# Optimization experiments

Measured on AMD Instinct MI355X. Metric: run time of the kernel, lower is better.

Reference implementation:

```python
import jax, jax.numpy as jnp
import numpy as np
from jax import lax

P, T, A = 4096, 128, 32
K = int(P * 0.1)          # elite count = 409
TEMP, MOM, MIN_STD = 0.5, 0.1, 0.05
INF = jnp.float32(1e30)   # large finite stand-in for +inf (grad-safe)


def setup_inputs() -> dict:
    key = jax.random.key(0)
    k1, k2 = jax.random.split(key)
    obs_diffs = jax.random.uniform(k1, (P, T, T), dtype=jnp.float32)  # pairwise MSE costs >= 0
    means = jnp.zeros((T, 1, A), dtype=jnp.float32)
    stds = jnp.ones((T, 1, A), dtype=jnp.float32)
    noise = jax.random.normal(k2, (T, P, A), dtype=jnp.float32)
    return {"obs_diffs": obs_diffs, "means": means, "stds": stds, "noise": noise}


def _dtw_dists(obs_diffs):
    """DTW-style min-plus DP: D[i+1,j+1] = min(D[i,j+1], D[i+1,j], D[i,j]) + c[i,j].
    obs_diffs: [P, T, T] -> dists: [P] (= D[:, T, T])."""
    p = obs_diffs.shape[0]
    inf_col = jnp.full((p,), INF, dtype=obs_diffs.dtype)
    # row 0 of the (T+1)x(T+1) table: [0, inf, inf, ...]
    row0 = jnp.concatenate([jnp.zeros((p, 1), obs_diffs.dtype),
                            jnp.full((p, obs_diffs.shape[1]), INF, obs_diffs.dtype)], axis=1)

    def row_step(prev_row, c_row):  # prev_row [P, T+1], c_row [P, T]
        def inner(carry, xs):        # carry = new[j] (left neighbor), vectorized over P
            p_j1, p_j, c = xs        # prev[j+1], prev[j], cost  -- each [P]
            new = jnp.minimum(jnp.minimum(p_j1, p_j), carry) + c
            return new, new
        xs = (prev_row[:, 1:].T, prev_row[:, :-1].T, c_row.T)  # each [T, P]
        _, vals = lax.scan(inner, inf_col, xs)                  # vals [T, P]
        new_row = jnp.concatenate([inf_col[:, None], vals.T], axis=1)
        return new_row, None

    final_row, _ = lax.scan(row_step, row0, jnp.swapaxes(obs_diffs, 0, 1))
    return final_row[:, -1]


def reference(obs_diffs, means, stds, noise):
    # sample population of action trajectories
    actions = jnp.clip(means + stds * noise, -1.0, 1.0)        # [T, P, A]
    dists = _dtw_dists(obs_diffs)                               # [P]
    neg_top, idxs = lax.top_k(-dists, K)                        # K smallest dists
    elite_diffs = -neg_top                                      # [K]
    elite_actions = actions[:, idxs]                            # [T, K, A]
    min_diff = elite_diffs.min()
    score = jnp.exp(TEMP * (min_diff - elite_diffs))
    score = score / score.sum()
    ssum = score.sum()                                          # == 1, kept to match torch
    w = score[None, :, None]                                    # [1, K, 1]
    _mean = jnp.sum(w * elite_actions, axis=1, keepdims=True) / (ssum + 1e-9)   # [T,1,A]
    _std = jnp.sqrt(jnp.sum(w * (elite_actions - _mean) ** 2, axis=1, keepdims=True) / (ssum + 1e-9))
    _std = jnp.clip(_std, MIN_STD, 1.0)
    means_new = MOM * means + (1.0 - MOM) * _mean
    return jnp.stack([means_new, _std])                         # [2, T, 1, A]
```

## Files before the change

kernel.cpp:

```cpp
#include <hip/hip_runtime.h>
#include <math.h>

#define P_N 4096
#define T_N 128
#define A_N 32
#define K_N 409
#define TEMP_C 0.5f
#define MOM_C 0.1f
#define MIN_STD_C 0.05f
#define INF_F 1e30f

typedef float vfloat4 __attribute__((ext_vector_type(4)));

#define DPPMOV(dst, src, ctrl, oldv)                                          \
  {                                                                           \
    union { float f; int i; } _a, _b, _r;                                     \
    _a.f = (src); _b.f = (oldv);                                              \
    _r.i = __builtin_amdgcn_update_dpp(_b.i, _a.i, (ctrl), 0xF, 0xF, false);  \
    (dst) = _r.f;                                                             \
  }

__global__ __launch_bounds__(256) void dtw_kernel(const float* __restrict__ obs,
                                                  float* __restrict__ dists) {
  const int tid  = threadIdx.x;
  const int wave = tid >> 6;
  const int lane = tid & 63;
  const int half = lane >> 5;
  const int l    = lane & 31;
  const int p    = blockIdx.x * 8 + wave * 2 + half;
  const bool is0 = (l == 0);

  const vfloat4* row = (const vfloat4*)(obs + (size_t)p * (T_N * T_N)) + l;

  float P1 = INF_F, P2 = INF_F, P3 = INF_F, P4 = INF_F;
  float p0 = is0 ? 0.0f : INF_F;

  vfloat4 cb[8];
  #pragma unroll
  for (int u = 0; u < 8; ++u) cb[u] = __builtin_nontemporal_load(row + u * 32);

  for (int rb = 0; rb < T_N; rb += 8) {
    const bool pf = (rb + 8 < T_N);
    #pragma unroll
    for (int u = 0; u < 8; ++u) {
      vfloat4 c = cb[u];
      if (pf) cb[u] = __builtin_nontemporal_load(row + (rb + u + 8) * 32);

      float a1 = fminf(P1, p0);
      float a2 = fminf(P2, P1);
      float a3 = fminf(P3, P2);
      float a4 = fminf(P4, P3);

      float B = a1 + c.x;
      B = fminf(B + c.y, a2 + c.y);
      B = fminf(B + c.z, a3 + c.z);
      B = fminf(B + c.w, a4 + c.w);
      float C = (c.x + c.y) + (c.z + c.w);

      float Bp, Cp;
      DPPMOV(Bp, B, 0x111, INF_F); DPPMOV(Cp, C, 0x111, 0.0f);
      B = fminf(Bp + C, B); C = Cp + C;
      DPPMOV(Bp, B, 0x112, INF_F); DPPMOV(Cp, C, 0x112, 0.0f);
      B = fminf(Bp + C, B); C = Cp + C;
      DPPMOV(Bp, B, 0x114, INF_F); DPPMOV(Cp, C, 0x114, 0.0f);
      B = fminf(Bp + C, B); C = Cp + C;
      DPPMOV(Bp, B, 0x118, INF_F); DPPMOV(Cp, C, 0x118, 0.0f);
      B = fminf(Bp + C, B); C = Cp + C;
      DPPMOV(Bp, B, 0x142, INF_F); DPPMOV(Cp, C, 0x142, 0.0f);
      B = fminf(Bp + C, B); C = Cp + C;

      float x;
      DPPMOV(x, B, 0x138, INF_F);
      x = is0 ? INF_F : x;

      float n1 = fminf(a1, x)  + c.x;
      float n2 = fminf(a2, n1) + c.y;
      float n3 = fminf(a3, n2) + c.z;
      float n4 = fminf(a4, n3) + c.w;

      p0 = x; P1 = n1; P2 = n2; P3 = n3; P4 = n4;
    }
  }

  if (l == 31) dists[p] = P4;
}

#define HSTRIDE 257

__global__ __launch_bounds__(1024) void select_kernel(const float* __restrict__ dists,
                                                      int* __restrict__ elite_idx,
                                                      float* __restrict__ elite_wn,
                                                      float* __restrict__ meta) {
  __shared__ alignas(16) unsigned int skey[P_N];
  __shared__ unsigned int histw[16 * HSTRIDE];
  __shared__ float elite_d[K_N];
  __shared__ int eqbuf[256];
  __shared__ float wsum[16];
  __shared__ unsigned int sc_prefix, sc_minkey;
  __shared__ int sc_r, sc_cntlt, sc_cnteq;
  __shared__ float sS, sS2;

  const int tid  = threadIdx.x;
  const int wid  = tid >> 6;
  const int lane = tid & 63;

  const float4 d4 = ((const float4*)dists)[tid];
  const unsigned int ka = __float_as_uint(d4.x);
  const unsigned int kb = __float_as_uint(d4.y);
  const unsigned int kc = __float_as_uint(d4.z);
  const unsigned int kd = __float_as_uint(d4.w);
  ((uint4*)skey)[tid] = make_uint4(ka, kb, kc, kd);
  unsigned int localmin = ka;
  if (kb < localmin) localmin = kb;
  if (kc < localmin) localmin = kc;
  if (kd < localmin) localmin = kd;
  #pragma unroll
  for (int d = 32; d > 0; d >>= 1) {
    unsigned int o = __shfl_xor(localmin, (unsigned)d, 64);
    if (o < localmin) localmin = o;
  }
  if (tid == 0) { sc_minkey = 0xFFFFFFFFu; sc_cntlt = 0; sc_cnteq = 0;
                  sc_prefix = 0; sc_r = K_N - 1; }
  __syncthreads();
  if (lane == 0) atomicMin(&sc_minkey, localmin);
  __syncthreads();

  unsigned int mask = 0;
  for (int shift = 24; shift >= 0; shift -= 8) {
    for (int b = tid; b < 16 * HSTRIDE; b += 1024) histw[b] = 0;
    __syncthreads();
    unsigned int pref = sc_prefix;
    for (int p = tid; p < P_N; p += 1024) {
      unsigned int k = skey[p];
      if ((k & mask) == pref)
        atomicAdd(&histw[wid * HSTRIDE + ((k >> shift) & 255u)], 1u);
    }
    __syncthreads();
    if (tid < 256) {
      unsigned tot = 0;
      #pragma unroll
      for (int w = 0; w < 16; ++w) tot += histw[w * HSTRIDE + tid];
      histw[tid] = tot;
    }
    __syncthreads();
    if (tid < 64) {
      unsigned h0 = histw[tid * 4 + 0], h1 = histw[tid * 4 + 1];
      unsigned h2 = histw[tid * 4 + 2], h3 = histw[tid * 4 + 3];
      unsigned s1 = h0 + h1, s2 = s1 + h2, s3 = s2 + h3;
      unsigned tot = s3;
      #pragma unroll
      for (int d = 1; d < 64; d <<= 1) {
        unsigned o = __shfl_up(tot, (unsigned)d, 64);
        if (tid >= d) tot += o;
      }
      unsigned base = tot - s3;
      unsigned rr = (unsigned)sc_r;
      if (rr >= base && rr < base + s3) {
        int bsel; unsigned lo;
        if (rr < base + h0)      { bsel = 0; lo = base; }
        else if (rr < base + s1) { bsel = 1; lo = base + h0; }
        else if (rr < base + s2) { bsel = 2; lo = base + s1; }
        else                     { bsel = 3; lo = base + s2; }
        sc_prefix |= (unsigned)(tid * 4 + bsel) << shift;
        sc_r = (int)(rr - lo);
      }
    }
    mask |= 0xFFu << shift;
    __syncthreads();
  }

  const unsigned int tk = sc_prefix;
  const int needeq = sc_r + 1;

  for (int p = tid; p < P_N; p += 1024) {
    unsigned int k = skey[p];
    const bool lt = (k < tk);
    unsigned long long m = __ballot(lt);
    int base = 0;
    if (lane == 0) base = atomicAdd(&sc_cntlt, (int)__popcll(m));
    base = __shfl(base, 0, 64);
    if (lt) {
      int pos = base + (int)__popcll(m & ((1ull << lane) - 1ull));
      elite_idx[pos] = p;
      elite_d[pos]   = __uint_as_float(k);
    } else if (k == tk) {
      int ep = atomicAdd(&sc_cnteq, 1);
      if (ep < 256) eqbuf[ep] = p;
    }
  }
  __syncthreads();
  if (tid == 0) {
    int cl = sc_cntlt;
    int ce = sc_cnteq; if (ce > 256) ce = 256;
    for (int rsel = 0; rsel < needeq; ++rsel) {
      int best = 0x7FFFFFFF, bi = 0;
      for (int m = 0; m < ce; ++m) {
        int v = eqbuf[m];
        if (v < best) { best = v; bi = m; }
      }
      eqbuf[bi] = 0x7FFFFFFF;
      elite_idx[cl + rsel] = best;
      elite_d[cl + rsel]   = __uint_as_float(tk);
    }
  }
  __syncthreads();

  const float minf = __uint_as_float(sc_minkey);
  float s = (tid < K_N) ? expf(TEMP_C * (minf - elite_d[tid])) : 0.0f;
  float t1 = s;
  #pragma unroll
  for (int d = 32; d > 0; d >>= 1) t1 += __shfl_xor(t1, (unsigned)d, 64);
  if (lane == 0) wsum[wid] = t1;
  __syncthreads();
  if (tid == 0) {
    float acc = 0.0f;
    #pragma unroll
    for (int w = 0; w < 16; ++w) acc += wsum[w];
    sS = acc;
  }
  __syncthreads();
  const float S = sS;
  const float wn = (tid < K_N) ? (s / S) : 0.0f;
  float t2 = wn;
  #pragma unroll
  for (int d = 32; d > 0; d >>= 1) t2 += __shfl_xor(t2, (unsigned)d, 64);
  if (lane == 0) wsum[wid] = t2;
  __syncthreads();
  if (tid == 0) {
    float acc = 0.0f;
    #pragma unroll
    for (int w = 0; w < 16; ++w) acc += wsum[w];
    sS2 = acc;
  }
  __syncthreads();
  if (tid < K_N) elite_wn[tid] = wn;
  if (tid == 0) meta[0] = sS2;
}

__global__ __launch_bounds__(512) void elite_stats_kernel(
    const float* __restrict__ noise, const float* __restrict__ means,
    const float* __restrict__ stds, const int* __restrict__ elite_idx,
    const float* __restrict__ elite_wn, const float* __restrict__ meta,
    float* __restrict__ out) {
  const int t = blockIdx.x;
  const int tid = threadIdx.x;
  const int a  = tid & 31;
  const int er = tid >> 5;
  __shared__ int   sidx[K_N];
  __shared__ float swn[K_N];
  __shared__ float sM[16][32];
  __shared__ float sQ[16][32];

  for (int e = tid; e < K_N; e += 512) { sidx[e] = elite_idx[e]; swn[e] = elite_wn[e]; }
  __syncthreads();

  const float mn = means[t * A_N + a];
  const float sd = stds[t * A_N + a];
  const float* nrow = noise + (size_t)t * P_N * A_N;

  float M = 0.0f, Q = 0.0f;
  for (int e = er; e < K_N; e += 16) {
    const int idx = sidx[e];
    const float w = swn[e];
    float x = mn + sd * nrow[idx * A_N + a];
    x = fminf(1.0f, fmaxf(-1.0f, x));
    M += w * x;
    Q += w * x * x;
  }
  sM[er][a] = M; sQ[er][a] = Q;
  __syncthreads();

  if (tid < 32) {
    float Ms = 0.0f, Qs = 0.0f;
    #pragma unroll
    for (int r = 0; r < 16; ++r) { Ms += sM[r][a]; Qs += sQ[r][a]; }
    const float ssum = meta[0];
    const float D = ssum + 1e-9f;
    const float mu = Ms / D;
    float var = (Qs - 2.0f * mu * Ms + mu * mu * ssum) / D;
    float stdv = sqrtf(fmaxf(var, 0.0f));
    stdv = fminf(1.0f, fmaxf(MIN_STD_C, stdv));
    out[t * A_N + a]              = MOM_C * mn + (1.0f - MOM_C) * mu;
    out[T_N * A_N + t * A_N + a]  = stdv;
  }
}

extern "C" void kernel_launch(void* const* d_in, const int* in_sizes, int n_in,
                              void* d_out, int out_size, void* d_ws, size_t ws_size,
                              hipStream_t stream) {
  const float* obs   = (const float*)d_in[0];
  const float* means = (const float*)d_in[1];
  const float* stds  = (const float*)d_in[2];
  const float* noise = (const float*)d_in[3];
  float* out = (float*)d_out;

  float* dists     = (float*)d_ws;
  int*   elite_idx = (int*)(dists + P_N);
  float* elite_wn  = (float*)(elite_idx + 512);
  float* meta      = elite_wn + 512;

  dtw_kernel<<<P_N / 8, 256, 0, stream>>>(obs, dists);
  select_kernel<<<1, 1024, 0, stream>>>(dists, elite_idx, elite_wn, meta);
  elite_stats_kernel<<<T_N, 512, 0, stream>>>(noise, means, stds,
                                              elite_idx, elite_wn, meta, out);
}
```

Measured before the change: 400.5 us.

## Fuse DTW, elite selection and stats into one flag-synchronized kernel

Merges the DTW, top-k selection and elite statistics kernels into a single launch of 256 blocks. Blocks hand off to each other through agent-scope done flags: the last block runs the selection once every DTW block has finished, and the first 128 blocks wait for it before computing the per-timestep stats. The radix select also skips leading bytes shared by the min and max keys, and uses ballot-aggregated histogram atomics. This removes inter-kernel launch gaps and some histogram work, but it depends on all blocks being co-resident and adds spin-wait overhead.

Result: slower. 533.9 us (+33.3%).

```diff
diff --git a/kernel.cpp b/kernel.cpp
--- a/kernel.cpp
+++ b/kernel.cpp
@@ -10,6 +10,14 @@
 #define MIN_STD_C 0.05f
 #define INF_F 1e30f
 
+#define NBLK 256
+#define NTHR 512
+#define NW   8
+#define HSTRIDE 257
+#define MAGIC_A 0x9E3779B1u
+#define MAGIC_B 0xC2B2AE35u
+#define SCOPE_AGT __HIP_MEMORY_SCOPE_AGENT
+
 typedef float vfloat4 __attribute__((ext_vector_type(4)));
 
 #define DPPMOV(dst, src, ctrl, oldv)                                          \
@@ -20,268 +28,322 @@
     (dst) = _r.f;                                                             \
   }
 
-__global__ __launch_bounds__(256) void dtw_kernel(const float* __restrict__ obs,
-                                                  float* __restrict__ dists) {
+union Shm {
+  struct {
+    unsigned int skey[P_N];
+    unsigned int histw[NW * HSTRIDE];
+    float elite_d[K_N];
+    int eqbuf[256];
+    float wsum[NW];
+  } sel;
+  struct {
+    int   sidx[K_N];
+    float swn[K_N];
+    float sM[16][32];
+    float sQ[16][32];
+  } st;
+};
+
+__global__ __launch_bounds__(NTHR, 2) void fused_kernel(
+    const float* __restrict__ obs, const float* __restrict__ means,
+    const float* __restrict__ stds, const float* __restrict__ noise,
+    float* __restrict__ dists, int* __restrict__ elite_idx,
+    float* __restrict__ elite_wn, float* __restrict__ meta,
+    unsigned int* __restrict__ done, float* __restrict__ out) {
+  __shared__ Shm shm;
+  __shared__ unsigned int sc_prefix, sc_minkey, sc_maxkey;
+  __shared__ int sc_r, sc_cntlt, sc_cnteq;
+  __shared__ float sS, sS2;
+
+  const int bid  = blockIdx.x;
   const int tid  = threadIdx.x;
   const int wave = tid >> 6;
   const int lane = tid & 63;
-  const int half = lane >> 5;
-  const int l    = lane & 31;
-  const int p    = blockIdx.x * 8 + wave * 2 + half;
-  const bool is0 = (l == 0);
-
-  const vfloat4* row = (const vfloat4*)(obs + (size_t)p * (T_N * T_N)) + l;
-
-  float P1 = INF_F, P2 = INF_F, P3 = INF_F, P4 = INF_F;
-  float p0 = is0 ? 0.0f : INF_F;
-
-  vfloat4 cb[8];
-  #pragma unroll
-  for (int u = 0; u < 8; ++u) cb[u] = __builtin_nontemporal_load(row + u * 32);
-
-  for (int rb = 0; rb < T_N; rb += 8) {
-    const bool pf = (rb + 8 < T_N);
+
+  {
+    const int half = lane >> 5;
+    const int l    = lane & 31;
+    const int p    = bid * 16 + wave * 2 + half;
+    const bool is0 = (l == 0);
+
+    const vfloat4* row = (const vfloat4*)(obs + (size_t)p * (T_N * T_N)) + l;
+
+    float P1 = INF_F, P2 = INF_F, P3 = INF_F, P4 = INF_F;
+    float p0 = is0 ? 0.0f : INF_F;
+
+    vfloat4 cb[8];
     #pragma unroll
-    for (int u = 0; u < 8; ++u) {
-      vfloat4 c = cb[u];
-      if (pf) cb[u] = __builtin_nontemporal_load(row + (rb + u + 8) * 32);
-
-      float a1 = fminf(P1, p0);
-      float a2 = fminf(P2, P1);
-      float a3 = fminf(P3, P2);
-      float a4 = fminf(P4, P3);
-
-      float B = a1 + c.x;
-      B = fminf(B + c.y, a2 + c.y);
-      B = fminf(B + c.z, a3 + c.z);
-      B = fminf(B + c.w, a4 + c.w);
-      float C = (c.x + c.y) + (c.z + c.w);
-
-      float Bp, Cp;
-      DPPMOV(Bp, B, 0x111, INF_F); DPPMOV(Cp, C, 0x111, 0.0f);
-      B = fminf(Bp + C, B); C = Cp + C;
-      DPPMOV(Bp, B, 0x112, INF_F); DPPMOV(Cp, C, 0x112, 0.0f);
-      B = fminf(Bp + C, B); C = Cp + C;
-      DPPMOV(Bp, B, 0x114, INF_F); DPPMOV(Cp, C, 0x114, 0.0f);
-      B = fminf(Bp + C, B); C = Cp + C;
-      DPPMOV(Bp, B, 0x118, INF_F); DPPMOV(Cp, C, 0x118, 0.0f);
-      B = fminf(Bp + C, B); C = Cp + C;
-      DPPMOV(Bp, B, 0x142, INF_F); DPPMOV(Cp, C, 0x142, 0.0f);
-      B = fminf(Bp + C, B); C = Cp + C;
-
-      float x;
-      DPPMOV(x, B, 0x138, INF_F);
-      x = is0 ? INF_F : x;
-
-      float n1 = fminf(a1, x)  + c.x;
-      float n2 = fminf(a2, n1) + c.y;
-      float n3 = fminf(a3, n2) + c.z;
-      float n4 = fminf(a4, n3) + c.w;
-
-      p0 = x; P1 = n1; P2 = n2; P3 = n3; P4 = n4;
-    }
+    for (int u = 0; u < 8; ++u) cb[u] = __builtin_nontemporal_load(row + u * 32);
+
+    for (int rb = 0; rb < T_N; rb += 8) {
+      const bool pf = (rb + 8 < T_N);
+      #pragma unroll
+      for (int u = 0; u < 8; ++u) {
+        vfloat4 c = cb[u];
+        if (pf) cb[u] = __builtin_nontemporal_load(row + (rb + u + 8) * 32);
+
+        float a1 = fminf(P1, p0);
+        float a2 = fminf(P2, P1);
+        float a3 = fminf(P3, P2);
+        float a4 = fminf(P4, P3);
+
+        float B = a1 + c.x;
+        B = fminf(B + c.y, a2 + c.y);
+        B = fminf(B + c.z, a3 + c.z);
+        B = fminf(B + c.w, a4 + c.w);
+        float C = (c.x + c.y) + (c.z + c.w);
+
+        float Bp, Cp;
+        DPPMOV(Bp, B, 0x111, INF_F); DPPMOV(Cp, C, 0x111, 0.0f);
+        B = fminf(Bp + C, B); C = Cp + C;
+        DPPMOV(Bp, B, 0x112, INF_F); DPPMOV(Cp, C, 0x112, 0.0f);
+        B = fminf(Bp + C, B); C = Cp + C;
+        DPPMOV(Bp, B, 0x114, INF_F); DPPMOV(Cp, C, 0x114, 0.0f);
+        B = fminf(Bp + C, B); C = Cp + C;
+        DPPMOV(Bp, B, 0x118, INF_F); DPPMOV(Cp, C, 0x118, 0.0f);
+        B = fminf(Bp + C, B); C = Cp + C;
+        DPPMOV(Bp, B, 0x142, INF_F); DPPMOV(Cp, C, 0x142, 0.0f);
+        B = fminf(Bp + C, B); C = Cp + C;
+
+        float x;
+        DPPMOV(x, B, 0x138, INF_F);
+        x = is0 ? INF_F : x;
+
+        float n1 = fminf(a1, x)  + c.x;
+        float n2 = fminf(a2, n1) + c.y;
+        float n3 = fminf(a3, n2) + c.z;
+        float n4 = fminf(a4, n3) + c.w;
+
+        p0 = x; P1 = n1; P2 = n2; P3 = n3; P4 = n4;
+      }
+    }
+    if (l == 31) dists[p] = P4;
   }
 
-  if (l == 31) dists[p] = P4;
-}
-
-#define HSTRIDE 257
-
-__global__ __launch_bounds__(1024) void select_kernel(const float* __restrict__ dists,
-                                                      int* __restrict__ elite_idx,
-                                                      float* __restrict__ elite_wn,
-                                                      float* __restrict__ meta) {
-  __shared__ alignas(16) unsigned int skey[P_N];
-  __shared__ unsigned int histw[16 * HSTRIDE];
-  __shared__ float elite_d[K_N];
-  __shared__ int eqbuf[256];
-  __shared__ float wsum[16];
-  __shared__ unsigned int sc_prefix, sc_minkey;
-  __shared__ int sc_r, sc_cntlt, sc_cnteq;
-  __shared__ float sS, sS2;
-
-  const int tid  = threadIdx.x;
-  const int wid  = tid >> 6;
-  const int lane = tid & 63;
-
-  const float4 d4 = ((const float4*)dists)[tid];
-  const unsigned int ka = __float_as_uint(d4.x);
-  const unsigned int kb = __float_as_uint(d4.y);
-  const unsigned int kc = __float_as_uint(d4.z);
-  const unsigned int kd = __float_as_uint(d4.w);
-  ((uint4*)skey)[tid] = make_uint4(ka, kb, kc, kd);
-  unsigned int localmin = ka;
-  if (kb < localmin) localmin = kb;
-  if (kc < localmin) localmin = kc;
-  if (kd < localmin) localmin = kd;
-  #pragma unroll
-  for (int d = 32; d > 0; d >>= 1) {
-    unsigned int o = __shfl_xor(localmin, (unsigned)d, 64);
-    if (o < localmin) localmin = o;
+  __threadfence();
+  __syncthreads();
+  if (tid == 0)
+    __hip_atomic_store(&done[bid], MAGIC_A, __ATOMIC_RELEASE, SCOPE_AGT);
+
+  if (bid == NBLK - 1) {
+    if (tid < NBLK) {
+      while (__hip_atomic_load(&done[tid], __ATOMIC_ACQUIRE, SCOPE_AGT) != MAGIC_A)
+        __builtin_amdgcn_s_sleep(8);
+    }
+    __syncthreads();
+    __threadfence();
+
+    if (tid == 0) { sc_minkey = 0xFFFFFFFFu; sc_maxkey = 0u;
+                    sc_cntlt = 0; sc_cnteq = 0; sc_prefix = 0u; sc_r = K_N - 1; }
+    __syncthreads();
+
+    unsigned int localmin = 0xFFFFFFFFu, localmax = 0u;
+    for (int p = tid; p < P_N; p += NTHR) {
+      float dv = __hip_atomic_load(&dists[p], __ATOMIC_RELAXED, SCOPE_AGT);
+      unsigned int k = __float_as_uint(dv);
+      shm.sel.skey[p] = k;
+      if (k < localmin) localmin = k;
+      if (k > localmax) localmax = k;
+    }
+    #pragma unroll
+    for (int d = 32; d > 0; d >>= 1) {
+      unsigned int o = __shfl_xor(localmin, (unsigned)d, 64);
+      if (o < localmin) localmin = o;
+      unsigned int o2 = __shfl_xor(localmax, (unsigned)d, 64);
+      if (o2 > localmax) localmax = o2;
+    }
+    if (lane == 0) { atomicMin(&sc_minkey, localmin); atomicMax(&sc_maxkey, localmax); }
+    __syncthreads();
+    const unsigned int mn = sc_minkey, mx = sc_maxkey;
+
+    unsigned int mask = 0;
+    bool skipping = true;
+    for (int shift = 24; shift >= 0; shift -= 8) {
+      const unsigned int bmin = (mn >> shift) & 255u;
+      const unsigned int bmax = (mx >> shift) & 255u;
+      if (skipping && bmin == bmax) {
+        if (tid == 0) sc_prefix |= bmin << shift;
+        mask |= 0xFFu << shift;
+        __syncthreads();
+        continue;
+      }
+      skipping = false;
+
+      for (int b = tid; b < NW * HSTRIDE; b += NTHR) shm.sel.histw[b] = 0u;
+      __syncthreads();
+      const unsigned int pref = sc_prefix;
+      for (int p = tid; p < P_N; p += NTHR) {
+        unsigned int k  = shm.sel.skey[p];
+        bool act        = ((k & mask) == pref);
+        unsigned int bk = (k >> shift) & 255u;
+        unsigned long long actm = __ballot(act);
+        #pragma unroll
+        for (int it = 0; it < 3; ++it) {
+          if (!actm) break;
+          int ldr = __ffsll((unsigned long long)actm) - 1;
+          unsigned int bl = __shfl(bk, ldr, 64);
+          unsigned long long mm = __ballot(act && (bk == bl));
+          if (act && (lane == ldr))
+            atomicAdd(&shm.sel.histw[wave * HSTRIDE + bl], (unsigned)__popcll(mm));
+          if (act && (bk == bl)) act = false;
+          actm &= ~mm;
+        }
+        if (act) atomicAdd(&shm.sel.histw[wave * HSTRIDE + bk], 1u);
+      }
+      __syncthreads();
+      if (tid < 256) {
+        unsigned int tot = 0;
+        #pragma unroll
+        for (int w = 0; w < NW; ++w) tot += shm.sel.histw[w * HSTRIDE + tid];
+        shm.sel.histw[tid] = tot;
+      }
+      __syncthreads();
+      if (tid < 64) {
+        unsigned h0 = shm.sel.histw[tid * 4 + 0], h1 = shm.sel.histw[tid * 4 + 1];
+        unsigned h2 = shm.sel.histw[tid * 4 + 2], h3 = shm.sel.histw[tid * 4 + 3];
+        unsigned s1 = h0 + h1, s2 = s1 + h2, s3 = s2 + h3;
+        unsigned tot = s3;
+        #pragma unroll
+        for (int d = 1; d < 64; d <<= 1) {
+          unsigned o = __shfl_up(tot, (unsigned)d, 64);
+          if (tid >= d) tot += o;
+        }
+        unsigned base = tot - s3;
+        unsigned rr = (unsigned)sc_r;
+        if (rr >= base && rr < base + s3) {
+          int bsel; unsigned lo;
+          if (rr < base + h0)      { bsel = 0; lo = base; }
+          else if (rr < base + s1) { bsel = 1; lo = base + h0; }
+          else if (rr < base + s2) { bsel = 2; lo = base + s1; }
+          else                     { bsel = 3; lo = base + s2; }
+          sc_prefix |= (unsigned)(tid * 4 + bsel) << shift;
+          sc_r = (int)(rr - lo);
+        }
+      }
+      mask |= 0xFFu << shift;
+      __syncthreads();
+    }
+
+    const unsigned int tk = sc_prefix;
+    const int needeq = sc_r + 1;
+
+    for (int p = tid; p < P_N; p += NTHR) {
+      unsigned int k = shm.sel.skey[p];
+      const bool lt = (k < tk);
+      unsigned long long m = __ballot(lt);
+      int base = 0;
+      if (lane == 0) base = atomicAdd(&sc_cntlt, (int)__popcll(m));
+      base = __shfl(base, 0, 64);
+      if (lt) {
+        int pos = base + (int)__popcll(m & ((1ull << lane) - 1ull));
+        elite_idx[pos]     = p;
+        shm.sel.elite_d[pos] = __uint_as_float(k);
+      } else if (k == tk) {
+        int ep = atomicAdd(&sc_cnteq, 1);
+        if (ep < 256) shm.sel.eqbuf[ep] = p;
+      }
+    }
+    __syncthreads();
+    if (tid == 0) {
+      int cl = sc_cntlt;
+      int ce = sc_cnteq; if (ce > 256) ce = 256;
+      for (int rsel = 0; rsel < needeq; ++rsel) {
+        int best = 0x7FFFFFFF, bi = 0;
+        for (int m = 0; m < ce; ++m) {
+          int v = shm.sel.eqbuf[m];
+          if (v < best) { best = v; bi = m; }
+        }
+        shm.sel.eqbuf[bi] = 0x7FFFFFFF;
+        elite_idx[cl + rsel]     = best;
+        shm.sel.elite_d[cl + rsel] = __uint_as_float(tk);
+      }
+    }
+    __syncthreads();
+
+    const float minf = __uint_as_float(sc_minkey);
+    float s = (tid < K_N) ? expf(TEMP_C * (minf - shm.sel.elite_d[tid])) : 0.0f;
+    float t1 = s;
+    #pragma unroll
+    for (int d = 32; d > 0; d >>= 1) t1 += __shfl_xor(t1, (unsigned)d, 64);
+    if (lane == 0) shm.sel.wsum[wave] = t1;
+    __syncthreads();
+    if (tid == 0) {
+      float acc = 0.0f;
+      #pragma unroll
+      for (int w = 0; w < NW; ++w) acc += shm.sel.wsum[w];
+      sS = acc;
+    }
+    __syncthreads();
+    const float S = sS;
+    const float wn = (tid < K_N) ? (s / S) : 0.0f;
+    float t2 = wn;
+    #pragma unroll
+    for (int d = 32; d > 0; d >>= 1) t2 += __shfl_xor(t2, (unsigned)d, 64);
+    if (lane == 0) shm.sel.wsum[wave] = t2;
+    __syncthreads();
+    if (tid == 0) {
+      float acc = 0.0f;
+      #pragma unroll
+      for (int w = 0; w < NW; ++w) acc += shm.sel.wsum[w];
+      sS2 = acc;
+    }
+    __syncthreads();
+    if (tid < K_N) elite_wn[tid] = wn;
+    if (tid == 0) meta[0] = sS2;
+
+    __threadfence();
+    __syncthreads();
+    if (tid < NBLK)
+      __hip_atomic_store(&done[tid], MAGIC_B, __ATOMIC_RELEASE, SCOPE_AGT);
   }
-  if (tid == 0) { sc_minkey = 0xFFFFFFFFu; sc_cntlt = 0; sc_cnteq = 0;
-                  sc_prefix = 0; sc_r = K_N - 1; }
-  __syncthreads();
-  if (lane == 0) atomicMin(&sc_minkey, localmin);
-  __syncthreads();
-
-  unsigned int mask = 0;
-  for (int shift = 24; shift >= 0; shift -= 8) {
-    for (int b = tid; b < 16 * HSTRIDE; b += 1024) histw[b] = 0;
-    __syncthreads();
-    unsigned int pref = sc_prefix;
-    for (int p = tid; p < P_N; p += 1024) {
-      unsigned int k = skey[p];
-      if ((k & mask) == pref)
-        atomicAdd(&histw[wid * HSTRIDE + ((k >> shift) & 255u)], 1u);
-    }
-    __syncthreads();
-    if (tid < 256) {
-      unsigned tot = 0;
+
+  if (bid < T_N) {
+    if (tid == 0) {
+      while (__hip_atomic_load(&done[bid], __ATOMIC_ACQUIRE, SCOPE_AGT) != MAGIC_B)
+        __builtin_amdgcn_s_sleep(8);
+    }
+    __syncthreads();
+    __threadfence();
+
+    const int t  = bid;
+    const int a  = tid & 31;
+    const int er = tid >> 5;
+
+    for (int e = tid; e < K_N; e += NTHR) {
+      shm.st.sidx[e] = __hip_atomic_load(&elite_idx[e], __ATOMIC_RELAXED, SCOPE_AGT);
+      shm.st.swn[e]  = __hip_atomic_load(&elite_wn[e],  __ATOMIC_RELAXED, SCOPE_AGT);
+    }
+    float ssum_l = __hip_atomic_load(&meta[0], __ATOMIC_RELAXED, SCOPE_AGT);
+    __syncthreads();
+
+    const float mn = means[t * A_N + a];
+    const float sd = stds[t * A_N + a];
+    const float* nrow = noise + (size_t)t * P_N * A_N;
+
+    float M = 0.0f, Q = 0.0f;
+    for (int e = er; e < K_N; e += 16) {
+      const int idx = shm.st.sidx[e];
+      const float w = shm.st.swn[e];
+      float x = mn + sd * nrow[idx * A_N + a];
+      x = fminf(1.0f, fmaxf(-1.0f, x));
+      M += w * x;
+      Q += w * x * x;
+    }
+    shm.st.sM[er][a] = M; shm.st.sQ[er][a] = Q;
+    __syncthreads();
+
+    if (tid < 32) {
+      float Ms = 0.0f, Qs = 0.0f;
       #pragma unroll
-      for (int w = 0; w < 16; ++w) tot += histw[w * HSTRIDE + tid];
-      histw[tid] = tot;
-    }
-    __syncthreads();
-    if (tid < 64) {
-      unsigned h0 = histw[tid * 4 + 0], h1 = histw[tid * 4 + 1];
-      unsigned h2 = histw[tid * 4 + 2], h3 = histw[tid * 4 + 3];
-      unsigned s1 = h0 + h1, s2 = s1 + h2, s3 = s2 + h3;
-      unsigned tot = s3;
-      #pragma unroll
-      for (int d = 1; d < 64; d <<= 1) {
-        unsigned o = __shfl_up(tot, (unsigned)d, 64);
-        if (tid >= d) tot += o;
-      }
-      unsigned base = tot - s3;
-      unsigned rr = (unsigned)sc_r;
-      if (rr >= base && rr < base + s3) {
-        int bsel; unsigned lo;
-        if (rr < base + h0)      { bsel = 0; lo = base; }
-        else if (rr < base + s1) { bsel = 1; lo = base + h0; }
-        else if (rr < base + s2) { bsel = 2; lo = base + s1; }
-        else                     { bsel = 3; lo = base + s2; }
-        sc_prefix |= (unsigned)(tid * 4 + bsel) << shift;
-        sc_r = (int)(rr - lo);
-      }
-    }
-    mask |= 0xFFu << shift;
-    __syncthreads();
-  }
-
-  const unsigned int tk = sc_prefix;
-  const int needeq = sc_r + 1;
-
-  for (int p = tid; p < P_N; p += 1024) {
-    unsigned int k = skey[p];
-    const bool lt = (k < tk);
-    unsigned long long m = __ballot(lt);
-    int base = 0;
-    if (lane == 0) base = atomicAdd(&sc_cntlt, (int)__popcll(m));
-    base = __shfl(base, 0, 64);
-    if (lt) {
-      int pos = base + (int)__popcll(m & ((1ull << lane) - 1ull));
-      elite_idx[pos] = p;
-      elite_d[pos]   = __uint_as_float(k);
-    } else if (k == tk) {
-      int ep = atomicAdd(&sc_cnteq, 1);
-      if (ep < 256) eqbuf[ep] = p;
-    }
-  }
-  __syncthreads();
-  if (tid == 0) {
-    int cl = sc_cntlt;
-    int ce = sc_cnteq; if (ce > 256) ce = 256;
-    for (int rsel = 0; rsel < needeq; ++rsel) {
-      int best = 0x7FFFFFFF, bi = 0;
-      for (int m = 0; m < ce; ++m) {
-        int v = eqbuf[m];
-        if (v < best) { best = v; bi = m; }
-      }
-      eqbuf[bi] = 0x7FFFFFFF;
-      elite_idx[cl + rsel] = best;
-      elite_d[cl + rsel]   = __uint_as_float(tk);
-    }
-  }
-  __syncthreads();
-
-  const float minf = __uint_as_float(sc_minkey);
-  float s = (tid < K_N) ? expf(TEMP_C * (minf - elite_d[tid])) : 0.0f;
-  float t1 = s;
-  #pragma unroll
-  for (int d = 32; d > 0; d >>= 1) t1 += __shfl_xor(t1, (unsigned)d, 64);
-  if (lane == 0) wsum[wid] = t1;
-  __syncthreads();
-  if (tid == 0) {
-    float acc = 0.0f;
-    #pragma unroll
-    for (int w = 0; w < 16; ++w) acc += wsum[w];
-    sS = acc;
-  }
-  __syncthreads();
-  const float S = sS;
-  const float wn = (tid < K_N) ? (s / S) : 0.0f;
-  float t2 = wn;
-  #pragma unroll
-  for (int d = 32; d > 0; d >>= 1) t2 += __shfl_xor(t2, (unsigned)d, 64);
-  if (lane == 0) wsum[wid] = t2;
-  __syncthreads();
-  if (tid == 0) {
-    float acc = 0.0f;
-    #pragma unroll
-    for (int w = 0; w < 16; ++w) acc += wsum[w];
-    sS2 = acc;
-  }
-  __syncthreads();
-  if (tid < K_N) elite_wn[tid] = wn;
-  if (tid == 0) meta[0] = sS2;
-}
-
-__global__ __launch_bounds__(512) void elite_stats_kernel(
-    const float* __restrict__ noise, const float* __restrict__ means,
-    const float* __restrict__ stds, const int* __restrict__ elite_idx,
-    const float* __restrict__ elite_wn, const float* __restrict__ meta,
-    float* __restrict__ out) {
-  const int t = blockIdx.x;
-  const int tid = threadIdx.x;
-  const int a  = tid & 31;
-  const int er = tid >> 5;
-  __shared__ int   sidx[K_N];
-  __shared__ float swn[K_N];
-  __shared__ float sM[16][32];
-  __shared__ float sQ[16][32];
-
-  for (int e = tid; e < K_N; e += 512) { sidx[e] = elite_idx[e]; swn[e] = elite_wn[e]; }
-  __syncthreads();
-
-  const float mn = means[t * A_N + a];
-  const float sd = stds[t * A_N + a];
-  const float* nrow = noise + (size_t)t * P_N * A_N;
-
-  float M = 0.0f, Q = 0.0f;
-  for (int e = er; e < K_N; e += 16) {
-    const int idx = sidx[e];
-    const float w = swn[e];
-    float x = mn + sd * nrow[idx * A_N + a];
-    x = fminf(1.0f, fmaxf(-1.0f, x));
-    M += w * x;
-    Q += w * x * x;
-  }
-  sM[er][a] = M; sQ[er][a] = Q;
-  __syncthreads();
-
-  if (tid < 32) {
-    float Ms = 0.0f, Qs = 0.0f;
-    #pragma unroll
-    for (int r = 0; r < 16; ++r) { Ms += sM[r][a]; Qs += sQ[r][a]; }
-    const float ssum = meta[0];
-    const float D = ssum + 1e-9f;
-    const float mu = Ms / D;
-    float var = (Qs - 2.0f * mu * Ms + mu * mu * ssum) / D;
-    float stdv = sqrtf(fmaxf(var, 0.0f));
-    stdv = fminf(1.0f, fmaxf(MIN_STD_C, stdv));
-    out[t * A_N + a]              = MOM_C * mn + (1.0f - MOM_C) * mu;
-    out[T_N * A_N + t * A_N + a]  = stdv;
+      for (int r = 0; r < 16; ++r) { Ms += shm.st.sM[r][a]; Qs += shm.st.sQ[r][a]; }
+      const float D = ssum_l + 1e-9f;
+      const float mu = Ms / D;
+      float var = (Qs - 2.0f * mu * Ms + mu * mu * ssum_l) / D;
+      float stdv = sqrtf(fmaxf(var, 0.0f));
+      stdv = fminf(1.0f, fmaxf(MIN_STD_C, stdv));
+      out[t * A_N + a]             = MOM_C * mn + (1.0f - MOM_C) * mu;
+      out[T_N * A_N + t * A_N + a] = stdv;
+    }
   }
 }
 
@@ -294,13 +356,13 @@
   const float* noise = (const float*)d_in[3];
   float* out = (float*)d_out;
 
-  float* dists     = (float*)d_ws;
-  int*   elite_idx = (int*)(dists + P_N);
-  float* elite_wn  = (float*)(elite_idx + 512);
-  float* meta      = elite_wn + 512;
-
-  dtw_kernel<<<P_N / 8, 256, 0, stream>>>(obs, dists);
-  select_kernel<<<1, 1024, 0, stream>>>(dists, elite_idx, elite_wn, meta);
-  elite_stats_kernel<<<T_N, 512, 0, stream>>>(noise, means, stds,
-                                              elite_idx, elite_wn, meta, out);
+  float* dists          = (float*)d_ws;
+  int*   elite_idx      = (int*)(dists + P_N);
+  float* elite_wn       = (float*)(elite_idx + 512);
+  float* meta           = elite_wn + 512;
+  unsigned int* done    = (unsigned int*)(meta + 16);
+
+  fused_kernel<<<NBLK, NTHR, 0, stream>>>(obs, means, stds, noise,
+                                          dists, elite_idx, elite_wn, meta,
+                                          done, out);
 }
```
